# Kernel tuning notes

Measured on AMD Instinct MI355X. Metric: run time of the kernel, lower is better.

Reference implementation:

```python
import jax, jax.numpy as jnp
import numpy as np

H = 128  # hidden_size == input_size

def setup_inputs() -> dict:
    key = jax.random.key(0)
    ks = jax.random.split(key, 8)
    T, B = 512, 1024
    s = 1.0 / np.sqrt(H)
    return {
        "input": jax.random.normal(ks[0], (T, B, H), dtype=jnp.float32),
        "initial_h": jax.random.normal(ks[1], (B, H), dtype=jnp.float32),
        "w_ih": jax.random.uniform(ks[2], (3 * H, H), jnp.float32, -s, s),
        "w_hh": jax.random.uniform(ks[3], (3 * H, H), jnp.float32, -s, s),
        "b_ih": jax.random.uniform(ks[4], (3 * H,), jnp.float32, -s, s),
        "b_hh": jax.random.uniform(ks[5], (3 * H,), jnp.float32, -s, s),
        "w_out": jax.random.uniform(ks[6], (1, H), jnp.float32, -s, s),
        "b_out": jax.random.uniform(ks[7], (1,), jnp.float32, -s, s),
    }

def reference(input, initial_h, w_ih, w_hh, b_ih, b_hh, w_out, b_out):
    # Pre-batch all input-to-hidden GEMMs: [T, B, 3H]
    xg = jnp.einsum("tbi,gi->tbg", input, w_ih) + b_ih

    def step(h, xg_t):
        hg = h @ w_hh.T + b_hh                       # [B, 3H]
        xr, xz, xn = jnp.split(xg_t, 3, axis=-1)
        hr, hz, hn = jnp.split(hg, 3, axis=-1)
        r = jax.nn.sigmoid(xr + hr)
        z = jax.nn.sigmoid(xz + hz)
        n = jnp.tanh(xn + r * hn)
        h_new = (1.0 - z) * n + z * h
        return h_new, None

    h, _ = jax.lax.scan(step, initial_h, xg)
    return h @ w_out.T + b_out                        # [B, 1]
```

## Files before the change

kernel.cpp:

```cpp
#include <hip/hip_runtime.h>

#define T_STEPS 512
#define BATCH   1024
#define HID     128

typedef __attribute__((ext_vector_type(8))) short short8;
typedef __attribute__((ext_vector_type(4))) float f32x4;

__device__ __forceinline__ unsigned cvtpk_bf16(float lo, float hi) {
    unsigned r;
    asm("v_cvt_pk_bf16_f32 %0, %1, %2" : "=v"(r) : "v"(lo), "v"(hi));
    return r;
}

__device__ __forceinline__ float fast_sigmoid(float x) {
    return __builtin_amdgcn_rcpf(1.0f + __builtin_amdgcn_exp2f(-1.442695041f * x));
}
__device__ __forceinline__ float fast_tanh(float x) {
    return 1.0f - 2.0f * __builtin_amdgcn_rcpf(1.0f + __builtin_amdgcn_exp2f(2.885390082f * x));
}

__device__ __forceinline__ float gru_el(float pr, float pz, float pxn, float phn, float h) {
    float r = fast_sigmoid(pr);
    float z = fast_sigmoid(pz);
    float n = fast_tanh(pxn + r * phn);
    return n + z * (h - n);
}

__global__ __launch_bounds__(512, 2) void gru_scan(
    const float* __restrict__ x, const float* __restrict__ h0,
    const float* __restrict__ w_ih, const float* __restrict__ w_hh,
    const float* __restrict__ b_ih, const float* __restrict__ b_hh,
    const float* __restrict__ w_out, const float* __restrict__ b_out,
    float* __restrict__ out)
{
    __shared__ float pre_r[16 * 132];
    __shared__ float pre_z[16 * 132];
    __shared__ float pre_xn[16 * 132];
    __shared__ float pre_hn[16 * 132];
    __shared__ float h32[16 * 132];
    __shared__ unsigned hbf[16 * 64];

    const int tid = threadIdx.x;
    const int w   = tid >> 6;
    const int l   = tid & 63;
    const int lm  = l & 15;
    const int lg  = l >> 4;
    const int b0  = blockIdx.x << 4;

    short8 wih[3][4], whh[3][4];
    float biasX[3], biasH[3];
    #pragma unroll
    for (int f = 0; f < 3; ++f) {
        const int n = w * 48 + f * 16 + lm;
        biasX[f] = b_ih[n];
        biasH[f] = b_hh[n];
        #pragma unroll
        for (int kf = 0; kf < 4; ++kf) {
            const int koff = kf * 32 + lg * 8;
            union { short8 s; unsigned u[4]; } p;
            {
                const float4 a = *(const float4*)(w_ih + n * HID + koff);
                const float4 b = *(const float4*)(w_ih + n * HID + koff + 4);
                p.u[0] = cvtpk_bf16(a.x, a.y); p.u[1] = cvtpk_bf16(a.z, a.w);
                p.u[2] = cvtpk_bf16(b.x, b.y); p.u[3] = cvtpk_bf16(b.z, b.w);
                wih[f][kf] = p.s;
            }
            {
                const float4 a = *(const float4*)(w_hh + n * HID + koff);
                const float4 b = *(const float4*)(w_hh + n * HID + koff + 4);
                p.u[0] = cvtpk_bf16(a.x, a.y); p.u[1] = cvtpk_bf16(a.z, a.w);
                p.u[2] = cvtpk_bf16(b.x, b.y); p.u[3] = cvtpk_bf16(b.z, b.w);
                whh[f][kf] = p.s;
            }
        }
    }

    {
        const int m  = tid >> 5;
        const int j0 = (tid & 31) << 2;
        const float4 hv = *(const float4*)(h0 + (b0 + m) * HID + j0);
        *(float4*)&h32[m * 132 + j0] = hv;
        const unsigned lo = cvtpk_bf16(hv.x, hv.y);
        const unsigned hi = cvtpk_bf16(hv.z, hv.w);
        const int bo = (j0 * 2) ^ ((m & 7) << 4);
        *(uint2*)&hbf[m * 64 + (bo >> 2)] = make_uint2(lo, hi);
    }

    float4 xnA[4], xnB[4];
    {
        const float* xr = x + (size_t)(b0 + lm) * HID;
        #pragma unroll
        for (int kf = 0; kf < 4; ++kf) {
            const int koff = kf * 32 + lg * 8;
            xnA[kf] = *(const float4*)(xr + koff);
            xnB[kf] = *(const float4*)(xr + koff + 4);
        }
    }

    __syncthreads();

    for (int t = 0; t < T_STEPS; ++t) {
        short8 xa[4];
        #pragma unroll
        for (int kf = 0; kf < 4; ++kf) {
            union { short8 s; unsigned u[4]; } p;
            p.u[0] = cvtpk_bf16(xnA[kf].x, xnA[kf].y);
            p.u[1] = cvtpk_bf16(xnA[kf].z, xnA[kf].w);
            p.u[2] = cvtpk_bf16(xnB[kf].x, xnB[kf].y);
            p.u[3] = cvtpk_bf16(xnB[kf].z, xnB[kf].w);
            xa[kf] = p.s;
        }
        {
            const int tn = (t < T_STEPS - 1) ? (t + 1) : t;
            const float* xr = x + ((size_t)tn * BATCH + b0 + lm) * HID;
            #pragma unroll
            for (int kf = 0; kf < 4; ++kf) {
                const int koff = kf * 32 + lg * 8;
                xnA[kf] = *(const float4*)(xr + koff);
                xnB[kf] = *(const float4*)(xr + koff + 4);
            }
        }
        short8 ha[4];
        #pragma unroll
        for (int kf = 0; kf < 4; ++kf) {
            const int bo = (kf * 64 + lg * 16) ^ ((lm & 7) << 4);
            ha[kf] = *(const short8*)&hbf[lm * 64 + (bo >> 2)];
        }
        f32x4 accX[3], accH[3];
        #pragma unroll
        for (int f = 0; f < 3; ++f) {
            accX[f] = (f32x4){biasX[f], biasX[f], biasX[f], biasX[f]};
            accH[f] = (f32x4){biasH[f], biasH[f], biasH[f], biasH[f]};
            #pragma unroll
            for (int kf = 0; kf < 4; ++kf) {
                accX[f] = __builtin_amdgcn_mfma_f32_16x16x32_bf16(xa[kf], wih[f][kf], accX[f], 0, 0, 0);
                accH[f] = __builtin_amdgcn_mfma_f32_16x16x32_bf16(ha[kf], whh[f][kf], accH[f], 0, 0, 0);
            }
        }
        #pragma unroll
        for (int f = 0; f < 3; ++f) {
            const int n0 = w * 48 + f * 16;
            const int n  = n0 + lm;
            if (n0 < 128) {
                #pragma unroll
                for (int r = 0; r < 4; ++r)
                    pre_r[(lg * 4 + r) * 132 + n] = accX[f][r] + accH[f][r];
            } else if (n0 < 256) {
                #pragma unroll
                for (int r = 0; r < 4; ++r)
                    pre_z[(lg * 4 + r) * 132 + (n - 128)] = accX[f][r] + accH[f][r];
            } else {
                #pragma unroll
                for (int r = 0; r < 4; ++r) {
                    pre_xn[(lg * 4 + r) * 132 + (n - 256)] = accX[f][r];
                    pre_hn[(lg * 4 + r) * 132 + (n - 256)] = accH[f][r];
                }
            }
        }
        __syncthreads();
        {
            const int m  = tid >> 5;
            const int j0 = (tid & 31) << 2;
            const float4 vr  = *(const float4*)&pre_r[m * 132 + j0];
            const float4 vz  = *(const float4*)&pre_z[m * 132 + j0];
            const float4 vxn = *(const float4*)&pre_xn[m * 132 + j0];
            const float4 vhn = *(const float4*)&pre_hn[m * 132 + j0];
            const float4 hold = *(const float4*)&h32[m * 132 + j0];
            float4 hnew;
            hnew.x = gru_el(vr.x, vz.x, vxn.x, vhn.x, hold.x);
            hnew.y = gru_el(vr.y, vz.y, vxn.y, vhn.y, hold.y);
            hnew.z = gru_el(vr.z, vz.z, vxn.z, vhn.z, hold.z);
            hnew.w = gru_el(vr.w, vz.w, vxn.w, vhn.w, hold.w);
            *(float4*)&h32[m * 132 + j0] = hnew;
            const unsigned lo = cvtpk_bf16(hnew.x, hnew.y);
            const unsigned hi = cvtpk_bf16(hnew.z, hnew.w);
            const int bo = (j0 * 2) ^ ((m & 7) << 4);
            *(uint2*)&hbf[m * 64 + (bo >> 2)] = make_uint2(lo, hi);
        }
        __syncthreads();
    }

    {
        const int m  = tid >> 5;
        const int j0 = (tid & 31) << 2;
        const float4 hv = *(const float4*)&h32[m * 132 + j0];
        const float4 wv = *(const float4*)(w_out + j0);
        float s = hv.x * wv.x + hv.y * wv.y + hv.z * wv.z + hv.w * wv.w;
        #pragma unroll
        for (int k = 16; k >= 1; k >>= 1) s += __shfl_xor(s, k, 32);
        if ((tid & 31) == 0) out[b0 + m] = s + b_out[0];
    }
}

extern "C" void kernel_launch(void* const* d_in, const int* in_sizes, int n_in,
                              void* d_out, int out_size, void* d_ws, size_t ws_size,
                              hipStream_t stream) {
    const float* x     = (const float*)d_in[0];
    const float* h0    = (const float*)d_in[1];
    const float* w_ih  = (const float*)d_in[2];
    const float* w_hh  = (const float*)d_in[3];
    const float* b_ih  = (const float*)d_in[4];
    const float* b_hh  = (const float*)d_in[5];
    const float* w_out = (const float*)d_in[6];
    const float* b_out = (const float*)d_in[7];
    gru_scan<<<64, 512, 0, stream>>>(x, h0, w_ih, w_hh, b_ih, b_hh, w_out, b_out, (float*)d_out);
}
```

Measured before the change: 1.170 ms.

## Fuse GRU gate math into MFMA epilogue with gate-aligned column mapping

Each wave now owns one 16-column slice across all three gates (r, z, n), so the GRU elementwise update runs straight from the MFMA accumulators in registers. The fp32 hidden state lives in registers, and the bf16 copy is double-buffered in LDS. This drops the preactivation LDS round trip and one of the two block barriers per timestep. In exchange, the bf16 hidden writes to LDS become scalar 16-bit stores, and the final output projection needs a cross-wave reduction.

```diff
diff --git a/kernel.cpp b/kernel.cpp
--- a/kernel.cpp
+++ b/kernel.cpp
@@ -20,13 +20,6 @@
     return 1.0f - 2.0f * __builtin_amdgcn_rcpf(1.0f + __builtin_amdgcn_exp2f(2.885390082f * x));
 }
 
-__device__ __forceinline__ float gru_el(float pr, float pz, float pxn, float phn, float h) {
-    float r = fast_sigmoid(pr);
-    float z = fast_sigmoid(pz);
-    float n = fast_tanh(pxn + r * phn);
-    return n + z * (h - n);
-}
-
 __global__ __launch_bounds__(512, 2) void gru_scan(
     const float* __restrict__ x, const float* __restrict__ h0,
     const float* __restrict__ w_ih, const float* __restrict__ w_hh,
@@ -34,12 +27,8 @@
     const float* __restrict__ w_out, const float* __restrict__ b_out,
     float* __restrict__ out)
 {
-    __shared__ float pre_r[16 * 132];
-    __shared__ float pre_z[16 * 132];
-    __shared__ float pre_xn[16 * 132];
-    __shared__ float pre_hn[16 * 132];
-    __shared__ float h32[16 * 132];
-    __shared__ unsigned hbf[16 * 64];
+    __shared__ unsigned hbf[2][16 * 64];
+    __shared__ float red[16][8];
 
     const int tid = threadIdx.x;
     const int w   = tid >> 6;
@@ -47,12 +36,13 @@
     const int lm  = l & 15;
     const int lg  = l >> 4;
     const int b0  = blockIdx.x << 4;
+    const int col = w * 16 + lm;
 
     short8 wih[3][4], whh[3][4];
     float biasX[3], biasH[3];
     #pragma unroll
     for (int f = 0; f < 3; ++f) {
-        const int n = w * 48 + f * 16 + lm;
+        const int n = f * 128 + col;
         biasX[f] = b_ih[n];
         biasH[f] = b_hh[n];
         #pragma unroll
@@ -76,15 +66,14 @@
         }
     }
 
-    {
-        const int m  = tid >> 5;
-        const int j0 = (tid & 31) << 2;
-        const float4 hv = *(const float4*)(h0 + (b0 + m) * HID + j0);
-        *(float4*)&h32[m * 132 + j0] = hv;
-        const unsigned lo = cvtpk_bf16(hv.x, hv.y);
-        const unsigned hi = cvtpk_bf16(hv.z, hv.w);
-        const int bo = (j0 * 2) ^ ((m & 7) << 4);
-        *(uint2*)&hbf[m * 64 + (bo >> 2)] = make_uint2(lo, hi);
+    float hreg[4];
+    #pragma unroll
+    for (int r = 0; r < 4; ++r) {
+        const int row = lg * 4 + r;
+        hreg[r] = h0[(size_t)(b0 + row) * HID + col];
+        const unsigned p = cvtpk_bf16(hreg[r], hreg[r]);
+        const int byte = (col * 2) ^ ((row & 7) << 4);
+        ((short*)hbf[0])[row * 128 + (byte >> 1)] = (short)p;
     }
 
     float4 xnA[4], xnB[4];
@@ -122,10 +111,13 @@
             }
         }
         short8 ha[4];
-        #pragma unroll
-        for (int kf = 0; kf < 4; ++kf) {
-            const int bo = (kf * 64 + lg * 16) ^ ((lm & 7) << 4);
-            ha[kf] = *(const short8*)&hbf[lm * 64 + (bo >> 2)];
+        {
+            const unsigned* hb = hbf[t & 1];
+            #pragma unroll
+            for (int kf = 0; kf < 4; ++kf) {
+                const int bo = (kf * 64 + lg * 16) ^ ((lm & 7) << 4);
+                ha[kf] = *(const short8*)&hb[lm * 64 + (bo >> 2)];
+            }
         }
         f32x4 accX[3], accH[3];
         #pragma unroll
@@ -138,58 +130,49 @@
                 accH[f] = __builtin_amdgcn_mfma_f32_16x16x32_bf16(ha[kf], whh[f][kf], accH[f], 0, 0, 0);
             }
         }
-        #pragma unroll
-        for (int f = 0; f < 3; ++f) {
-            const int n0 = w * 48 + f * 16;
-            const int n  = n0 + lm;
-            if (n0 < 128) {
-                #pragma unroll
-                for (int r = 0; r < 4; ++r)
-                    pre_r[(lg * 4 + r) * 132 + n] = accX[f][r] + accH[f][r];
-            } else if (n0 < 256) {
-                #pragma unroll
-                for (int r = 0; r < 4; ++r)
-                    pre_z[(lg * 4 + r) * 132 + (n - 128)] = accX[f][r] + accH[f][r];
-            } else {
-                #pragma unroll
-                for (int r = 0; r < 4; ++r) {
-                    pre_xn[(lg * 4 + r) * 132 + (n - 256)] = accX[f][r];
-                    pre_hn[(lg * 4 + r) * 132 + (n - 256)] = accH[f][r];
-                }
+        {
+            short* hw = (short*)hbf[(t + 1) & 1];
+            #pragma unroll
+            for (int r = 0; r < 4; ++r) {
+                const int row = lg * 4 + r;
+                const float pr = accX[0][r] + accH[0][r];
+                const float pz = accX[1][r] + accH[1][r];
+                const float rr = fast_sigmoid(pr);
+                const float zz = fast_sigmoid(pz);
+                const float nn = fast_tanh(accX[2][r] + rr * accH[2][r]);
+                const float hn = nn + zz * (hreg[r] - nn);
+                hreg[r] = hn;
+                const unsigned p = cvtpk_bf16(hn, hn);
+                const int byte = (col * 2) ^ ((row & 7) << 4);
+                hw[row * 128 + (byte >> 1)] = (short)p;
             }
-        }
-        __syncthreads();
-        {
-            const int m  = tid >> 5;
-            const int j0 = (tid & 31) << 2;
-            const float4 vr  = *(const float4*)&pre_r[m * 132 + j0];
-            const float4 vz  = *(const float4*)&pre_z[m * 132 + j0];
-            const float4 vxn = *(const float4*)&pre_xn[m * 132 + j0];
-            const float4 vhn = *(const float4*)&pre_hn[m * 132 + j0];
-            const float4 hold = *(const float4*)&h32[m * 132 + j0];
-            float4 hnew;
-            hnew.x = gru_el(vr.x, vz.x, vxn.x, vhn.x, hold.x);
-            hnew.y = gru_el(vr.y, vz.y, vxn.y, vhn.y, hold.y);
-            hnew.z = gru_el(vr.z, vz.z, vxn.z, vhn.z, hold.z);
-            hnew.w = gru_el(vr.w, vz.w, vxn.w, vhn.w, hold.w);
-            *(float4*)&h32[m * 132 + j0] = hnew;
-            const unsigned lo = cvtpk_bf16(hnew.x, hnew.y);
-            const unsigned hi = cvtpk_bf16(hnew.z, hnew.w);
-            const int bo = (j0 * 2) ^ ((m & 7) << 4);
-            *(uint2*)&hbf[m * 64 + (bo >> 2)] = make_uint2(lo, hi);
         }
         __syncthreads();
     }
 
     {
-        const int m  = tid >> 5;
-        const int j0 = (tid & 31) << 2;
-        const float4 hv = *(const float4*)&h32[m * 132 + j0];
-        const float4 wv = *(const float4*)(w_out + j0);
-        float s = hv.x * wv.x + hv.y * wv.y + hv.z * wv.z + hv.w * wv.w;
+        const float wv = w_out[col];
+        float s0 = hreg[0] * wv, s1 = hreg[1] * wv, s2 = hreg[2] * wv, s3 = hreg[3] * wv;
         #pragma unroll
-        for (int k = 16; k >= 1; k >>= 1) s += __shfl_xor(s, k, 32);
-        if ((tid & 31) == 0) out[b0 + m] = s + b_out[0];
+        for (int mask = 8; mask >= 1; mask >>= 1) {
+            s0 += __shfl_xor(s0, mask);
+            s1 += __shfl_xor(s1, mask);
+            s2 += __shfl_xor(s2, mask);
+            s3 += __shfl_xor(s3, mask);
+        }
+        if (lm == 0) {
+            red[lg * 4 + 0][w] = s0;
+            red[lg * 4 + 1][w] = s1;
+            red[lg * 4 + 2][w] = s2;
+            red[lg * 4 + 3][w] = s3;
+        }
+    }
+    __syncthreads();
+    if (tid < 16) {
+        float acc = b_out[0];
+        #pragma unroll
+        for (int j = 0; j < 8; ++j) acc += red[tid][j];
+        out[b0 + tid] = acc;
     }
 }
 
```

After: 1.166 ms. About the same (-0.3%).
